# Optimization experiments

Hardware: AMD Instinct MI355X
Metric: run time of the kernel (lower is better)

## Reference

```python
import jax, jax.numpy as jnp
import numpy as np

NUM_HEADS = 16


def setup_inputs() -> dict:
    key = jax.random.key(0)
    k1, k2, k3 = jax.random.split(key, 3)
    B, N, C = 2, 2048, 1024
    x = jax.random.normal(k1, (B, N, C), dtype=jnp.float32)
    w_qkv = jax.random.normal(k2, (3 * C, C), dtype=jnp.float32) * (C ** -0.5)
    w_proj = jax.random.normal(k3, (C, C), dtype=jnp.float32) * (C ** -0.5)
    b_proj = jnp.zeros((C,), dtype=jnp.float32)
    return {"x": x, "w_qkv": w_qkv, "w_proj": w_proj, "b_proj": b_proj}


def reference(x, w_qkv, w_proj, b_proj):
    B, N, C = x.shape
    H = NUM_HEADS
    D = C // H
    scale = 1.0 / jnp.sqrt(jnp.asarray(D, x.dtype))
    qkv = (x @ w_qkv.T).reshape(B, N, 3, H, D)
    qkv = jnp.transpose(qkv, (2, 0, 3, 1, 4))  # [3,B,H,N,D]
    q, k, v = qkv[0], qkv[1], qkv[2]
    # scaled dot-product attention with explicit score matrix [B,H,N,N]
    attn = jnp.einsum('bhnd,bhmd->bhnm', q, k) * scale
    attn = jax.nn.softmax(attn, axis=-1)
    out = jnp.einsum('bhnm,bhmd->bhnd', attn, v)
    out = jnp.transpose(out, (0, 2, 1, 3)).reshape(B, N, C)
    # output projection
    return out @ w_proj.T + b_proj
```

## Files before the change

### kernel.cpp

```cpp
#include <hip/hip_runtime.h>

typedef unsigned short u16;
typedef __attribute__((ext_vector_type(8))) short bf16x8;
typedef __attribute__((ext_vector_type(4))) float f32x4;
typedef __attribute__((ext_vector_type(16))) float f32x16;
typedef __attribute__((ext_vector_type(4))) unsigned u32x4;

#define B_ 2
#define N_ 2048
#define C_ 1024
#define H_ 16
#define D_ 64
#define M_ (B_ * N_)

#define QSCALE 0.18033688011114336f

#define EXP2R(x) __builtin_amdgcn_exp2f(x)

__device__ __forceinline__ u16 f2bf(float f) {
    union { float f; unsigned u; } x; x.f = f;
    return (u16)((x.u + 0x8000u) >> 16);
}
__device__ __forceinline__ unsigned pack2bf(float a, float b) {
    union { float f; unsigned u; } x, y; x.f = a; y.f = b;
    return __builtin_amdgcn_perm(y.u + 0x8000u, x.u + 0x8000u, 0x07060302);
}
__device__ __forceinline__ unsigned cvtpk2bf(float a, float b) {
    unsigned r;
    asm("v_cvt_pk_bf16_f32 %0, %1, %2" : "=v"(r) : "v"(a), "v"(b));
    return r;
}

__device__ __forceinline__ void async_copy16(const void* gsrc, void* ldst) {
    __builtin_amdgcn_global_load_lds(
        (__attribute__((address_space(1))) void*)gsrc,
        (__attribute__((address_space(3))) void*)ldst,
        16, 0, 0);
}

__global__ void cast3_kernel(const float* __restrict__ x, const float* __restrict__ wq,
                             const float* __restrict__ wp, u16* __restrict__ xo,
                             u16* __restrict__ wqo, u16* __restrict__ wpo) {
    int b = blockIdx.x;
    const float* s; u16* d;
    if (b < 4096)      { s = x;  d = xo;  }
    else if (b < 7168) { s = wq; d = wqo; b -= 4096; }
    else               { s = wp; d = wpo; b -= 7168; }
    int i = (b * 256 + threadIdx.x) * 4;
    const float4 v = *(const float4*)(s + i);
    uint2 o;
    o.x = pack2bf(v.x, v.y);
    o.y = pack2bf(v.z, v.w);
    *(uint2*)(d + i) = o;
}

__global__ __launch_bounds__(256, 3) void gemm_qkv(
    const u16* __restrict__ A, const u16* __restrict__ Bm,
    u16* __restrict__ qo, u16* __restrict__ ko, u16* __restrict__ vt) {
    __shared__ u16 As[128 * 64];
    __shared__ u16 Bs[128 * 64];
    const int K = C_, ntiles_n = 24;
    const int tid = threadIdx.x, lane = tid & 63, w = tid >> 6;
    const int cpx = gridDim.x >> 3;
    const int sbid = (blockIdx.x & 7) * cpx + (blockIdx.x >> 3);
    const int bx = sbid % ntiles_n, by = sbid / ntiles_n;
    const int m0 = by * 128, n0 = bx * 128;
    const int wm = w >> 1, wn = w & 1;
    const int q16 = lane >> 4, l15 = lane & 15;
    const int r0 = lane >> 3, c0 = (lane & 7) * 8;
    f32x4 acc[4][4] = {};

    for (int k0 = 0; k0 < K; k0 += 64) {
#pragma unroll
        for (int i = 0; i < 4; ++i) {
            int blk = w * 4 + i;
            int r = blk * 8 + r0;
            async_copy16(A + (size_t)(m0 + r) * K + k0 + c0, (char*)As + blk * 1024);
            async_copy16(Bm + (size_t)(n0 + r) * K + k0 + c0, (char*)Bs + blk * 1024);
        }
        __builtin_amdgcn_s_waitcnt(0);
        __syncthreads();
#pragma unroll
        for (int ks = 0; ks < 2; ++ks) {
            bf16x8 af[4], bf[4];
#pragma unroll
            for (int i = 0; i < 4; ++i) {
                af[i] = *(const bf16x8*)&As[(wm * 64 + i * 16 + l15) * 64 + ks * 32 + q16 * 8];
                bf[i] = *(const bf16x8*)&Bs[(wn * 64 + i * 16 + l15) * 64 + ks * 32 + q16 * 8];
            }
#pragma unroll
            for (int mi = 0; mi < 4; ++mi)
#pragma unroll
                for (int ni = 0; ni < 4; ++ni)
                    acc[mi][ni] = __builtin_amdgcn_mfma_f32_16x16x32_bf16(af[mi], bf[ni], acc[mi][ni], 0, 0, 0);
        }
        __syncthreads();
    }

#pragma unroll
    for (int mi = 0; mi < 4; ++mi) {
#pragma unroll
        for (int ni = 0; ni < 4; ++ni) {
            int n_g = n0 + wn * 64 + ni * 16 + l15;
            int which = n_g >> 10;
            int h = (n_g >> 6) & 15;
            int d = n_g & 63;
            int m_base = m0 + wm * 64 + mi * 16 + q16 * 4;
            int b = m_base >> 11;
            int nn0 = m_base & 2047;
            if (which == 2) {
                uint2 pk;
                pk.x = pack2bf(acc[mi][ni][0], acc[mi][ni][1]);
                pk.y = pack2bf(acc[mi][ni][2], acc[mi][ni][3]);
                *(uint2*)(vt + ((size_t)((b * H_ + h) * D_ + d) << 11) + nn0) = pk;
            } else {
                size_t base = ((size_t)((b * H_ + h) * N_ + nn0) << 6) + d;
#pragma unroll
                for (int r = 0; r < 4; ++r) {
                    float v = acc[mi][ni][r];
                    if (which == 0) qo[base + (size_t)r * D_] = f2bf(v * QSCALE);
                    else            ko[base + (size_t)r * D_] = f2bf(v);
                }
            }
        }
    }
}

__global__ __launch_bounds__(256, 2) void gemm_out(
    const u16* __restrict__ A, const u16* __restrict__ Bm,
    const float* __restrict__ bias, float* __restrict__ out) {
    __shared__ u16 As[128 * 64];
    __shared__ u16 Bs[64 * 64];
    const int K = C_, Ncols = C_, ntiles_n = 16;
    const int tid = threadIdx.x, lane = tid & 63, w = tid >> 6;
    const int cpx = gridDim.x >> 3;
    const int sbid = (blockIdx.x & 7) * cpx + (blockIdx.x >> 3);
    const int bx = sbid % ntiles_n, by = sbid / ntiles_n;
    const int m0 = by * 128, n0 = bx * 64;
    const int wm = w >> 1, wn = w & 1;
    const int q16 = lane >> 4, l15 = lane & 15;
    const int r0 = lane >> 3, c0 = (lane & 7) * 8;
    f32x4 acc[4][2] = {};

    for (int k0 = 0; k0 < K; k0 += 64) {
#pragma unroll
        for (int i = 0; i < 4; ++i) {
            int blk = w * 4 + i;
            int r = blk * 8 + r0;
            async_copy16(A + (size_t)(m0 + r) * K + k0 + c0, (char*)As + blk * 1024);
        }
#pragma unroll
        for (int i = 0; i < 2; ++i) {
            int blk = w * 2 + i;
            int r = blk * 8 + r0;
            async_copy16(Bm + (size_t)(n0 + r) * K + k0 + c0, (char*)Bs + blk * 1024);
        }
        __builtin_amdgcn_s_waitcnt(0);
        __syncthreads();
#pragma unroll
        for (int ks = 0; ks < 2; ++ks) {
            bf16x8 af[4], bf[2];
#pragma unroll
            for (int i = 0; i < 4; ++i)
                af[i] = *(const bf16x8*)&As[(wm * 64 + i * 16 + l15) * 64 + ks * 32 + q16 * 8];
#pragma unroll
            for (int i = 0; i < 2; ++i)
                bf[i] = *(const bf16x8*)&Bs[(wn * 32 + i * 16 + l15) * 64 + ks * 32 + q16 * 8];
#pragma unroll
            for (int mi = 0; mi < 4; ++mi)
#pragma unroll
                for (int ni = 0; ni < 2; ++ni)
                    acc[mi][ni] = __builtin_amdgcn_mfma_f32_16x16x32_bf16(af[mi], bf[ni], acc[mi][ni], 0, 0, 0);
        }
        __syncthreads();
    }

#pragma unroll
    for (int mi = 0; mi < 4; ++mi) {
#pragma unroll
        for (int ni = 0; ni < 2; ++ni) {
            int n_g = n0 + wn * 32 + ni * 16 + l15;
#pragma unroll
            for (int r = 0; r < 4; ++r) {
                int m_g = m0 + wm * 64 + mi * 16 + q16 * 4 + r;
                out[(size_t)m_g * Ncols + n_g] = acc[mi][ni][r] + bias[n_g];
            }
        }
    }
}

__global__ __launch_bounds__(512, 1) void attn_kernel(
    const u16* __restrict__ Q, const u16* __restrict__ K,
    const u16* __restrict__ VT, u16* __restrict__ O) {
    __shared__ u16 Ks[2][2][64 * 64];
    __shared__ u16 Vs[2][2][64 * 64];
    const int tid = threadIdx.x, lane = tid & 63, w = tid >> 6;
    const int l31 = lane & 31, hi = lane >> 5, l7 = l31 & 7;
    const int bid = blockIdx.x;
    const int bh = (bid & 7) * 4 + (bid >> 6);
    const int q0 = ((bid >> 3) & 7) * 256;
    const size_t head = (size_t)bh * N_ * D_;
    const int lr3 = lane >> 3, lc7 = lane & 7;

    auto stage = [&](int kt, int buf) {
        int key0 = kt * 128;
        int row = w * 8 + lr3;
#pragma unroll
        for (int s = 0; s < 2; ++s) {
            async_copy16(K + head + (size_t)(key0 + s * 64 + row) * D_ + (lc7 ^ lr3) * 8,
                         (char*)Ks[buf][s] + w * 1024);
            async_copy16(VT + head + (size_t)row * N_ + key0 + s * 64 + (lc7 ^ lr3) * 8,
                         (char*)Vs[buf][s] + w * 1024);
        }
    };

    bf16x8 qf[4];
#pragma unroll
    for (int ds = 0; ds < 4; ++ds)
        qf[ds] = *(const bf16x8*)(Q + head + (size_t)(q0 + w * 32 + l31) * D_ + ds * 16 + hi * 8);
    stage(0, 0);
    __builtin_amdgcn_s_waitcnt(0);
    __syncthreads();

    f32x16 o_acc[2] = {};
    float rs = 0.f;

    for (int kt = 0; kt < 16; ++kt) {
        int buf = kt & 1;
        stage((kt + 1) & 15, buf ^ 1);

#pragma unroll
        for (int s = 0; s < 2; ++s) {
#pragma unroll
            for (int kb2 = 0; kb2 < 2; ++kb2) {
                f32x16 st = {};
                __builtin_amdgcn_s_setprio(1);
#pragma unroll
                for (int ds = 0; ds < 4; ++ds) {
                    bf16x8 kf = *(const bf16x8*)&Ks[buf][s][(kb2 * 32 + l31) * 64 + ((ds * 2 + hi) ^ l7) * 8];
                    st = __builtin_amdgcn_mfma_f32_32x32x16_bf16(kf, qf[ds], st, 0, 0, 0);
                }
                __builtin_amdgcn_s_setprio(0);

                float p[16];
#pragma unroll
                for (int i = 0; i < 16; ++i) p[i] = EXP2R(st[i]);
#pragma unroll
                for (int i = 0; i < 16; ++i) rs += p[i];

                unsigned a0 = cvtpk2bf(p[0], p[1]),   b0 = cvtpk2bf(p[4], p[5]);
                unsigned a1 = cvtpk2bf(p[2], p[3]),   b1 = cvtpk2bf(p[6], p[7]);
                unsigned a2 = cvtpk2bf(p[8], p[9]),   b2 = cvtpk2bf(p[12], p[13]);
                unsigned a3 = cvtpk2bf(p[10], p[11]), b3 = cvtpk2bf(p[14], p[15]);
                asm("v_permlane32_swap_b32 %0, %1" : "+v"(a0), "+v"(b0));
                asm("v_permlane32_swap_b32 %0, %1" : "+v"(a1), "+v"(b1));
                asm("v_permlane32_swap_b32 %0, %1" : "+v"(a2), "+v"(b2));
                asm("v_permlane32_swap_b32 %0, %1" : "+v"(a3), "+v"(b3));
                union { u32x4 u; bf16x8 v; } af0, af1;
                af0.u = (u32x4){a0, a1, b0, b1};
                af1.u = (u32x4){a2, a3, b2, b3};

                __builtin_amdgcn_s_setprio(1);
#pragma unroll
                for (int db = 0; db < 2; ++db) {
                    bf16x8 vf0 = *(const bf16x8*)&Vs[buf][s][(db * 32 + l31) * 64 + ((kb2 * 4 + hi) ^ l7) * 8];
                    o_acc[db] = __builtin_amdgcn_mfma_f32_32x32x16_bf16(af0.v, vf0, o_acc[db], 0, 0, 0);
                    bf16x8 vf1 = *(const bf16x8*)&Vs[buf][s][(db * 32 + l31) * 64 + ((kb2 * 4 + 2 + hi) ^ l7) * 8];
                    o_acc[db] = __builtin_amdgcn_mfma_f32_32x32x16_bf16(af1.v, vf1, o_acc[db], 0, 0, 0);
                }
                __builtin_amdgcn_s_setprio(0);
            }
        }

        __builtin_amdgcn_s_waitcnt(0);
        __syncthreads();
    }

    rs += __shfl_xor(rs, 32);
    float rsi = 1.0f / rs;

    const int b = bh >> 4, h = bh & 15;
#pragma unroll
    for (int reg = 0; reg < 16; ++reg) {
        int qrow = (reg & 3) + 8 * (reg >> 2) + 4 * hi;
        float inv = __shfl(rsi, qrow);
        int qg = q0 + w * 32 + qrow;
#pragma unroll
        for (int db = 0; db < 2; ++db) {
            int d = db * 32 + l31;
            O[((size_t)(b * N_ + qg) << 10) + h * 64 + d] = f2bf(o_acc[db][reg] * inv);
        }
    }
}

extern "C" void kernel_launch(void* const* d_in, const int* in_sizes, int n_in,
                              void* d_out, int out_size, void* d_ws, size_t ws_size,
                              hipStream_t stream) {
    const float* x      = (const float*)d_in[0];
    const float* w_qkv  = (const float*)d_in[1];
    const float* w_proj = (const float*)d_in[2];
    const float* b_proj = (const float*)d_in[3];
    float* out = (float*)d_out;

    char* ws = (char*)d_ws;
    const size_t MB = 1024 * 1024;
    u16* x_bf     = (u16*)(ws + 0 * MB);
    u16* wqkv_bf  = (u16*)(ws + 8 * MB);
    u16* wproj_bf = (u16*)(ws + 14 * MB);
    u16* q_bf     = (u16*)(ws + 16 * MB);
    u16* k_bf     = (u16*)(ws + 24 * MB);
    u16* vt_bf    = (u16*)(ws + 32 * MB);
    u16* ao_bf    = (u16*)(ws + 40 * MB);

    cast3_kernel<<<8192, 256, 0, stream>>>(x, w_qkv, w_proj, x_bf, wqkv_bf, wproj_bf);

    gemm_qkv<<<768, 256, 0, stream>>>(x_bf, wqkv_bf, q_bf, k_bf, vt_bf);

    attn_kernel<<<256, 512, 0, stream>>>(q_bf, k_bf, vt_bf, ao_bf);

    gemm_out<<<512, 256, 0, stream>>>(ao_bf, wproj_bf, b_proj, out);
}
```

Before: 178.8 us.

## Rewrite QKV GEMM as 256x256 8-wave double-buffered pipelined kernel

Replaces the 128x128 single-buffered QKV GEMM with a 256x256 tile computed by 8 waves. The K loop is split into half-tile stages, double-buffered in LDS with an XOR-swizzled layout, and async loads are interleaved with MFMA bursts under fine-grained barriers and raised priority. The goal is to hide global load latency, avoid LDS bank conflicts and raise arithmetic intensity per tile. The trade-off is only 192 blocks on a 256-CU device, more registers for the larger accumulator, and many barriers.

```diff
diff --git a/kernel.cpp b/kernel.cpp
--- a/kernel.cpp
+++ b/kernel.cpp
@@ -54,70 +54,132 @@
     *(uint2*)(d + i) = o;
 }
 
-__global__ __launch_bounds__(256, 3) void gemm_qkv(
+__global__ __launch_bounds__(512, 2) void gemm_qkv8(
     const u16* __restrict__ A, const u16* __restrict__ Bm,
     u16* __restrict__ qo, u16* __restrict__ ko, u16* __restrict__ vt) {
-    __shared__ u16 As[128 * 64];
-    __shared__ u16 Bs[128 * 64];
-    const int K = C_, ntiles_n = 24;
+    __shared__ u16 L[2][4][8192];
     const int tid = threadIdx.x, lane = tid & 63, w = tid >> 6;
-    const int cpx = gridDim.x >> 3;
-    const int sbid = (blockIdx.x & 7) * cpx + (blockIdx.x >> 3);
-    const int bx = sbid % ntiles_n, by = sbid / ntiles_n;
-    const int m0 = by * 128, n0 = bx * 128;
-    const int wm = w >> 1, wn = w & 1;
-    const int q16 = lane >> 4, l15 = lane & 15;
-    const int r0 = lane >> 3, c0 = (lane & 7) * 8;
-    f32x4 acc[4][4] = {};
-
-    for (int k0 = 0; k0 < K; k0 += 64) {
+    const int wm = w >> 2, wn = w & 3;
+    const int q16 = lane >> 4, l15 = lane & 15, l7 = lane & 7;
+    const int lr3 = lane >> 3, lc7 = lane & 7;
+    const int sbid = (blockIdx.x & 7) * 24 + (blockIdx.x >> 3);
+    const int bx = sbid % 12, by = sbid / 12;
+    const int m0 = by * 256, n0 = bx * 256;
+    const int cswz8 = (lc7 ^ lr3) * 8;
+
+    auto stageHT = [&](int t, int isB, int h) {
+        if (t > 15) return;
+        const u16* src = isB ? Bm : A;
+        int base_row = (isB ? n0 : m0) + h * 128;
+#pragma unroll
+        for (int i = 0; i < 2; ++i) {
+            int c = w * 2 + i;
+            async_copy16(src + (size_t)(base_row + c * 8 + lr3) * 1024 + t * 64 + cswz8,
+                         (char*)L + ((t & 1) * 4 + isB * 2 + h) * 16384 + c * 1024);
+        }
+    };
+
+    stageHT(0, 0, 0); stageHT(0, 1, 0); stageHT(0, 1, 1); stageHT(0, 0, 1);
+    stageHT(1, 0, 0); stageHT(1, 1, 0); stageHT(1, 1, 1);
+    asm volatile("s_waitcnt vmcnt(6)" ::: "memory");
+    __builtin_amdgcn_s_barrier();
+
+    f32x4 acc[8][4] = {};
+    const int aRow = l15 * 64;
+    const int colsw0 = (q16 ^ l7) * 8, colsw1 = ((4 + q16) ^ l7) * 8;
+    const u16* LA[2] = { &L[0][wm][0], &L[1][wm][0] };
+    const u16* LB[2] = { &L[0][2 + (wn >> 1)][0], &L[1][2 + (wn >> 1)][0] };
+    const int bOff = (wn & 1) * 4096;
+
+    bf16x8 Af[4][2], Bf0[2][2], Bf1[2][2];
+
+    auto readA = [&](int P, int mh) {
 #pragma unroll
         for (int i = 0; i < 4; ++i) {
-            int blk = w * 4 + i;
-            int r = blk * 8 + r0;
-            async_copy16(A + (size_t)(m0 + r) * K + k0 + c0, (char*)As + blk * 1024);
-            async_copy16(Bm + (size_t)(n0 + r) * K + k0 + c0, (char*)Bs + blk * 1024);
-        }
-        __builtin_amdgcn_s_waitcnt(0);
-        __syncthreads();
-#pragma unroll
-        for (int ks = 0; ks < 2; ++ks) {
-            bf16x8 af[4], bf[4];
-#pragma unroll
-            for (int i = 0; i < 4; ++i) {
-                af[i] = *(const bf16x8*)&As[(wm * 64 + i * 16 + l15) * 64 + ks * 32 + q16 * 8];
-                bf[i] = *(const bf16x8*)&Bs[(wn * 64 + i * 16 + l15) * 64 + ks * 32 + q16 * 8];
-            }
-#pragma unroll
-            for (int mi = 0; mi < 4; ++mi)
-#pragma unroll
-                for (int ni = 0; ni < 4; ++ni)
-                    acc[mi][ni] = __builtin_amdgcn_mfma_f32_16x16x32_bf16(af[mi], bf[ni], acc[mi][ni], 0, 0, 0);
-        }
-        __syncthreads();
-    }
-
-#pragma unroll
-    for (int mi = 0; mi < 4; ++mi) {
-#pragma unroll
-        for (int ni = 0; ni < 4; ++ni) {
-            int n_g = n0 + wn * 64 + ni * 16 + l15;
+            Af[i][0] = *(const bf16x8*)(LA[P] + (mh * 64 + i * 16) * 64 + aRow + colsw0);
+            Af[i][1] = *(const bf16x8*)(LA[P] + (mh * 64 + i * 16) * 64 + aRow + colsw1);
+        }
+    };
+    auto readB = [&](int P, int nh, bf16x8 (*Bf)[2]) {
+#pragma unroll
+        for (int j = 0; j < 2; ++j) {
+            Bf[j][0] = *(const bf16x8*)(LB[P] + bOff + (nh * 32 + j * 16) * 64 + aRow + colsw0);
+            Bf[j][1] = *(const bf16x8*)(LB[P] + bOff + (nh * 32 + j * 16) * 64 + aRow + colsw1);
+        }
+    };
+    auto mfma16 = [&](int mh, int nh, bf16x8 (*Bf)[2]) {
+        __builtin_amdgcn_s_setprio(1);
+#pragma unroll
+        for (int i = 0; i < 4; ++i)
+#pragma unroll
+            for (int j = 0; j < 2; ++j)
+#pragma unroll
+                for (int ks = 0; ks < 2; ++ks)
+                    acc[mh * 4 + i][nh * 2 + j] = __builtin_amdgcn_mfma_f32_16x16x32_bf16(
+                        Af[i][ks], Bf[j][ks], acc[mh * 4 + i][nh * 2 + j], 0, 0, 0);
+        __builtin_amdgcn_s_setprio(0);
+    };
+
+    for (int it = 0; it < 8; ++it) {
+        const int T = 2 * it;
+        readA(0, 0); readB(0, 0, Bf0); stageHT(T + 1, 0, 1);
+        __builtin_amdgcn_s_barrier();
+        mfma16(0, 0, Bf0);
+        __builtin_amdgcn_s_barrier();
+        readB(0, 1, Bf1);
+        __builtin_amdgcn_s_barrier();
+        mfma16(0, 1, Bf1);
+        __builtin_amdgcn_s_barrier();
+        readA(0, 1); stageHT(T + 2, 1, 0);
+        __builtin_amdgcn_s_barrier();
+        mfma16(1, 1, Bf1);
+        __builtin_amdgcn_s_barrier();
+        stageHT(T + 2, 1, 1); stageHT(T + 2, 0, 0);
+        __builtin_amdgcn_s_barrier();
+        mfma16(1, 0, Bf0);
+        if (it < 7) { asm volatile("s_waitcnt vmcnt(6)" ::: "memory"); }
+        else        { asm volatile("s_waitcnt vmcnt(0)" ::: "memory"); }
+        __builtin_amdgcn_s_barrier();
+        readA(1, 0); readB(1, 0, Bf0); stageHT(T + 2, 0, 1);
+        __builtin_amdgcn_s_barrier();
+        mfma16(0, 0, Bf0);
+        __builtin_amdgcn_s_barrier();
+        readB(1, 1, Bf1);
+        __builtin_amdgcn_s_barrier();
+        mfma16(0, 1, Bf1);
+        __builtin_amdgcn_s_barrier();
+        readA(1, 1); stageHT(T + 3, 1, 0);
+        __builtin_amdgcn_s_barrier();
+        mfma16(1, 1, Bf1);
+        __builtin_amdgcn_s_barrier();
+        stageHT(T + 3, 1, 1); stageHT(T + 3, 0, 0);
+        __builtin_amdgcn_s_barrier();
+        mfma16(1, 0, Bf0);
+        if (it < 7) { asm volatile("s_waitcnt vmcnt(6)" ::: "memory"); }
+        __builtin_amdgcn_s_barrier();
+    }
+
+#pragma unroll
+    for (int fm = 0; fm < 8; ++fm) {
+#pragma unroll
+        for (int fn = 0; fn < 4; ++fn) {
+            int n_g = n0 + wn * 64 + fn * 16 + l15;
             int which = n_g >> 10;
             int h = (n_g >> 6) & 15;
             int d = n_g & 63;
-            int m_base = m0 + wm * 64 + mi * 16 + q16 * 4;
+            int m_base = m0 + wm * 128 + fm * 16 + q16 * 4;
             int b = m_base >> 11;
             int nn0 = m_base & 2047;
             if (which == 2) {
                 uint2 pk;
-                pk.x = pack2bf(acc[mi][ni][0], acc[mi][ni][1]);
-                pk.y = pack2bf(acc[mi][ni][2], acc[mi][ni][3]);
+                pk.x = pack2bf(acc[fm][fn][0], acc[fm][fn][1]);
+                pk.y = pack2bf(acc[fm][fn][2], acc[fm][fn][3]);
                 *(uint2*)(vt + ((size_t)((b * H_ + h) * D_ + d) << 11) + nn0) = pk;
             } else {
                 size_t base = ((size_t)((b * H_ + h) * N_ + nn0) << 6) + d;
 #pragma unroll
                 for (int r = 0; r < 4; ++r) {
-                    float v = acc[mi][ni][r];
+                    float v = acc[fm][fn][r];
                     if (which == 0) qo[base + (size_t)r * D_] = f2bf(v * QSCALE);
                     else            ko[base + (size_t)r * D_] = f2bf(v);
                 }
@@ -314,7 +376,7 @@
 
     cast3_kernel<<<8192, 256, 0, stream>>>(x, w_qkv, w_proj, x_bf, wqkv_bf, wproj_bf);
 
-    gemm_qkv<<<768, 256, 0, stream>>>(x_bf, wqkv_bf, q_bf, k_bf, vt_bf);
+    gemm_qkv8<<<192, 512, 0, stream>>>(x_bf, wqkv_bf, q_bf, k_bf, vt_bf);
 
     attn_kernel<<<256, 512, 0, stream>>>(q_bf, k_bf, vt_bf, ao_bf);
 
```

New measurement: 175.4 us. No clear change (-1.9%).
